# Kernel optimization log

Measured on AMD Instinct MI355X. Metric: run time of the kernel, lower is better.

Reference implementation:

```python
import jax, jax.numpy as jnp
import numpy as np

N = 100000   # num_nodes
F_IN = 128   # num_features
D = 64       # encoder_dim
E = 1600000  # num raw edges (avg degree 16)
BETA = 0.01  # perturb_value


def setup_inputs() -> dict:
    key = jax.random.key(0)
    ks = jax.random.split(key, 8)
    x = jax.random.normal(ks[0], (N, F_IN), dtype=jnp.float32)
    edge_index = jax.random.randint(ks[1], (2, E), 0, N, dtype=jnp.int64)
    W1 = jax.random.normal(ks[2], (F_IN, D), dtype=jnp.float32) * 0.05
    b1 = jnp.zeros((D,), dtype=jnp.float32)
    W2 = jax.random.normal(ks[3], (D, D), dtype=jnp.float32) * 0.05
    b2 = jnp.zeros((D,), dtype=jnp.float32)
    # torch FloatTensor(...).normal_(-beta, beta): mean=-beta, std=beta
    perturb1 = jax.random.normal(ks[4], (N, D), dtype=jnp.float32) * BETA - BETA
    perturb2 = jax.random.normal(ks[5], (N, D), dtype=jnp.float32) * BETA - BETA
    return {"x": x, "edge_index": edge_index, "W1": W1, "b1": b1,
            "W2": W2, "b2": b2, "perturb1": perturb1, "perturb2": perturb2}


def _graph_conv(h, src, dst, norm, W, b):
    # linear transform then gather -> weighted message -> scatter-add
    h = h @ W                                  # [N, D]
    msg = h[src] * norm[:, None]               # [E+N, D] irregular gather
    agg = jax.ops.segment_sum(msg, dst, num_segments=N)  # scatter-add
    return agg + b


def reference(x, edge_index, W1, b1, W2, b2, perturb1, perturb2):
    # add self-loops (GCN/PPMI-style propagation with symmetric norm;
    # PPMI edge weights approximated by degree normalization)
    loops = jnp.arange(N, dtype=edge_index.dtype)
    src = jnp.concatenate([edge_index[0], loops])
    dst = jnp.concatenate([edge_index[1], loops])
    deg = jax.ops.segment_sum(jnp.ones_like(dst, dtype=x.dtype), dst, num_segments=N)
    deg = jnp.maximum(deg, 1.0)
    norm = jax.lax.rsqrt(deg[src] * deg[dst])  # [E+N]

    h = _graph_conv(x, src, dst, norm, W1, b1) + perturb1
    h = jax.nn.relu(h)                         # dropout = identity (eval mode)
    h = _graph_conv(h, src, dst, norm, W2, b2) + perturb2
    return h
```

## Files before the change

### kernel.cpp

```cpp
#include <hip/hip_runtime.h>

#define DD 64
#define FIN 128
#define BK 256
#define MAXBUK 512
#define CAP 8192
#define ESCAP 12288
#define EPB 4096

typedef _Float16 half8 __attribute__((ext_vector_type(8)));
typedef _Float16 h2 __attribute__((ext_vector_type(2)));
typedef float f32x4 __attribute__((ext_vector_type(4)));

union U4 { uint4 u; h2 h[4]; };

__global__ __launch_bounds__(256) void k_bucket(const int* __restrict__ src,
                                                const int* __restrict__ dst,
                                                unsigned* __restrict__ buf,
                                                int* __restrict__ gcur,
                                                int E, int nbuk) {
    __shared__ int hist[MAXBUK];
    __shared__ int base[MAXBUK];
    int e0 = blockIdx.x * EPB;
    int e1 = min(e0 + EPB, E);
    int dreg[16];
#pragma unroll
    for (int i = 0; i < 16; ++i) {
        int e = e0 + threadIdx.x + i * 256;
        dreg[i] = (e < e1) ? dst[e] : -1;
    }
    for (int i = threadIdx.x; i < nbuk; i += 256) hist[i] = 0;
    __syncthreads();
#pragma unroll
    for (int i = 0; i < 16; ++i)
        if (dreg[i] >= 0) atomicAdd(&hist[dreg[i] >> 8], 1);
    __syncthreads();
    for (int i = threadIdx.x; i < nbuk; i += 256) {
        int c = hist[i];
        base[i] = c ? atomicAdd(&gcur[i], c) : 0;
        hist[i] = 0;
    }
    __syncthreads();
#pragma unroll
    for (int i = 0; i < 16; ++i) {
        int d = dreg[i];
        if (d >= 0) {
            int e = e0 + threadIdx.x + i * 256;
            int b = d >> 8;
            int off = base[b] + atomicAdd(&hist[b], 1);
            if (off < CAP)
                buf[(size_t)b * CAP + off] = ((unsigned)src[e] << 8) | ((unsigned)d & 255u);
        }
    }
}

__global__ __launch_bounds__(256) void k_csr(const unsigned* __restrict__ buf,
                                             const int* __restrict__ gcur,
                                             int* __restrict__ rowptr,
                                             int* __restrict__ lenp,
                                             float* __restrict__ rs,
                                             int* __restrict__ es, int n, int dummy) {
    __shared__ int cnt[BK];
    __shared__ int excl[BK];
    __shared__ int cur[BK];
    __shared__ int wsum[4];
    int b = blockIdx.x;
    int tid = threadIdx.x;
    int lane = tid & 63, wid = tid >> 6;
    cnt[tid] = 0;
    cur[tid] = 0;
    __syncthreads();
    int count = gcur[b];
    const unsigned* rec = buf + (size_t)b * CAP;
    for (int i = tid; i < count; i += 256)
        atomicAdd(&cnt[rec[i] & (BK - 1)], 1);
    __syncthreads();
    int v = cnt[tid];
    int pv = (v + 15) & ~15;
    int s = pv;
    for (int off = 1; off < 64; off <<= 1) {
        int t = __shfl_up(s, off, 64);
        if (lane >= off) s += t;
    }
    if (lane == 63) wsum[wid] = s;
    __syncthreads();
    int wo = 0;
    for (int w = 0; w < wid; ++w) wo += wsum[w];
    excl[tid] = s - pv + wo;
    __syncthreads();
    int node = b * BK + tid;
    int base = b * ESCAP;
    if (node < n) {
        rowptr[node] = base + excl[tid];
        lenp[node] = pv;
        rs[node] = rsqrtf((float)(v + 1));
    }
    for (int i = tid; i < count; i += 256) {
        unsigned r = rec[i];
        int local = r & (BK - 1);
        int pos = base + excl[local] + atomicAdd(&cur[local], 1);
        es[pos] = (int)(r >> 8);
    }
    int st = base + excl[tid];
    for (int i = v; i < pv; ++i) es[st + i] = dummy;
}

__global__ __launch_bounds__(256) void k_prep(const float* __restrict__ W1,
                                              const float* __restrict__ W2,
                                              _Float16* __restrict__ Wt1,
                                              _Float16* __restrict__ Wt2,
                                              int* __restrict__ gcur) {
    int tid = threadIdx.x;
    gcur[tid] = 0;
    gcur[tid + 256] = 0;
    for (int i = tid; i < FIN * DD; i += 256) {
        int k = i >> 6, c = i & 63;
        Wt1[c * FIN + k] = (_Float16)W1[i];
    }
    for (int i = tid; i < DD * DD; i += 256) {
        int k = i >> 6, c = i & 63;
        Wt2[c * DD + k] = (_Float16)W2[i];
    }
}

__global__ __launch_bounds__(256) void k_gemm1(const float* __restrict__ x,
                                               const _Float16* __restrict__ Wt,
                                               const float* __restrict__ rs,
                                               _Float16* __restrict__ hpf, int n) {
    __shared__ _Float16 sx[64 * 136];
    int row0 = blockIdx.x * 64;
    int tid = threadIdx.x;
    for (int i = tid; i < 2048; i += 256) {
        int r = i >> 5, c = i & 31;
        int row = row0 + r;
        float4 v = make_float4(0.f, 0.f, 0.f, 0.f);
        if (row < n) v = *(const float4*)(x + (size_t)row * FIN + c * 4);
        union { _Float16 h[4]; uint2 u; } t;
        t.h[0] = (_Float16)v.x; t.h[1] = (_Float16)v.y;
        t.h[2] = (_Float16)v.z; t.h[3] = (_Float16)v.w;
        *(uint2*)(sx + r * 136 + c * 4) = t.u;
    }
    __syncthreads();
    int lane = tid & 63, wave = tid >> 6;
    int r15 = lane & 15, g = lane >> 4;
    half8 a[4];
    const _Float16* ap = sx + (wave * 16 + r15) * 136 + g * 8;
#pragma unroll
    for (int kc = 0; kc < 4; ++kc) a[kc] = *(const half8*)(ap + kc * 32);
    half8 bfr[4][4];
    const _Float16* bp = Wt + (size_t)r15 * FIN + g * 8;
#pragma unroll
    for (int ct = 0; ct < 4; ++ct)
#pragma unroll
        for (int kc = 0; kc < 4; ++kc)
            bfr[ct][kc] = *(const half8*)(bp + ct * 16 * FIN + kc * 32);
    f32x4 acc[4] = {{0.f,0.f,0.f,0.f},{0.f,0.f,0.f,0.f},{0.f,0.f,0.f,0.f},{0.f,0.f,0.f,0.f}};
#pragma unroll
    for (int ct = 0; ct < 4; ++ct)
#pragma unroll
        for (int kc = 0; kc < 4; ++kc)
            acc[ct] = __builtin_amdgcn_mfma_f32_16x16x32_f16(a[kc], bfr[ct][kc], acc[ct], 0, 0, 0);
    __syncthreads();
#pragma unroll
    for (int reg = 0; reg < 4; ++reg) {
        int rowl = wave * 16 + g * 4 + reg;
        int row = row0 + rowl;
        float sc = (row < n) ? rs[row] : 0.f;
#pragma unroll
        for (int ct = 0; ct < 4; ++ct)
            sx[rowl * 72 + ct * 16 + r15] = (_Float16)(acc[ct][reg] * sc);
    }
    __syncthreads();
    for (int i = tid; i < 1024; i += 256) {
        int r = i >> 4, q = i & 15;
        uint2 v = *(const uint2*)(sx + r * 72 + q * 4);
        *(uint2*)(hpf + (size_t)(row0 + r) * DD + q * 4) = v;
    }
}

#define GATHER_BODY                                                              \
    int e0 = rowptr[nc];                                                         \
    int len = alive ? lenp[nc] : 0;                                              \
    int nbt = len >> 4;                                                          \
    h2 ac[2][2][4] = {};                                                         \
    {                                                                            \
        U4 t0, t1;                                                               \
        t0.u = hp4[(size_t)nc * 8 + q];                                          \
        t1.u = hp4[(size_t)nc * 8 + q + 4];                                      \
        _Pragma("unroll")                                                        \
        for (int k = 0; k < 4; ++k) { ac[0][0][k] += t0.h[k]; ac[1][0][k] += t1.h[k]; } \
    }                                                                            \
    for (int t = 0; t < nbt; ++t) {                                              \
        uint4 eb = *(const uint4*)(es + e0 + t * 16 + q * 4);                    \
        int jj[16];                                                              \
        _Pragma("unroll")                                                        \
        for (int l = 0; l < 4; ++l) {                                            \
            jj[l]      = __shfl((int)eb.x, l, 4);                                \
            jj[4 + l]  = __shfl((int)eb.y, l, 4);                                \
            jj[8 + l]  = __shfl((int)eb.z, l, 4);                                \
            jj[12 + l] = __shfl((int)eb.w, l, 4);                                \
        }                                                                        \
        _Pragma("unroll")                                                        \
        for (int hb = 0; hb < 2; ++hb) {                                         \
            U4 v0[8], v1[8];                                                     \
            _Pragma("unroll")                                                    \
            for (int m = 0; m < 8; ++m) {                                        \
                size_t bb = (size_t)jj[hb * 8 + m] * 8;                          \
                v0[m].u = hp4[bb + q];                                           \
                v1[m].u = hp4[bb + q + 4];                                       \
            }                                                                    \
            _Pragma("unroll")                                                    \
            for (int m = 0; m < 8; ++m) {                                        \
                _Pragma("unroll")                                                \
                for (int k = 0; k < 4; ++k) {                                    \
                    ac[0][m & 1][k] += v0[m].h[k];                               \
                    ac[1][m & 1][k] += v1[m].h[k];                               \
                }                                                                \
            }                                                                    \
        }                                                                        \
    }                                                                            \
    float F0[8], F1[8];                                                          \
    _Pragma("unroll")                                                            \
    for (int k = 0; k < 4; ++k) {                                                \
        F0[2 * k]     = (float)ac[0][0][k].x + (float)ac[0][1][k].x;             \
        F0[2 * k + 1] = (float)ac[0][0][k].y + (float)ac[0][1][k].y;             \
        F1[2 * k]     = (float)ac[1][0][k].x + (float)ac[1][1][k].x;             \
        F1[2 * k + 1] = (float)ac[1][0][k].y + (float)ac[1][1][k].y;             \
    }

__global__ __launch_bounds__(256) void k_aggemm(const uint4* __restrict__ hp4,
                                                const int* __restrict__ es,
                                                const int* __restrict__ rowptr,
                                                const int* __restrict__ lenp,
                                                const float* __restrict__ rs,
                                                const float* __restrict__ b,
                                                const float* __restrict__ pert,
                                                const _Float16* __restrict__ Wt,
                                                _Float16* __restrict__ hpo, int n) {
    __shared__ _Float16 sx[64 * 72];
    int tid = threadIdx.x;
    int lane = tid & 63, wv = tid >> 6;
    int q = lane & 3, g = lane >> 2;
    int row0 = blockIdx.x * 64;
    int rowl = wv * 16 + g;
    int node = row0 + rowl;
    bool alive = node < n;
    int nc = alive ? node : 0;
    GATHER_BODY
    {
        float r = rs[nc];
        size_t op = (size_t)nc * DD + q * 8;
        float4 p0 = *(const float4*)(pert + op);
        float4 p1 = *(const float4*)(pert + op + 4);
        float4 p2 = *(const float4*)(pert + op + 32);
        float4 p3 = *(const float4*)(pert + op + 36);
        float4 b0 = *(const float4*)(b + q * 8);
        float4 b1 = *(const float4*)(b + q * 8 + 4);
        float4 b2 = *(const float4*)(b + q * 8 + 32);
        float4 b3 = *(const float4*)(b + q * 8 + 36);
        union { _Float16 h[8]; uint4 u; } t0, t1;
        float m = alive ? 1.f : 0.f;
        t0.h[0] = (_Float16)(m * fmaxf(fmaf(r, F0[0], b0.x + p0.x), 0.f));
        t0.h[1] = (_Float16)(m * fmaxf(fmaf(r, F0[1], b0.y + p0.y), 0.f));
        t0.h[2] = (_Float16)(m * fmaxf(fmaf(r, F0[2], b0.z + p0.z), 0.f));
        t0.h[3] = (_Float16)(m * fmaxf(fmaf(r, F0[3], b0.w + p0.w), 0.f));
        t0.h[4] = (_Float16)(m * fmaxf(fmaf(r, F0[4], b1.x + p1.x), 0.f));
        t0.h[5] = (_Float16)(m * fmaxf(fmaf(r, F0[5], b1.y + p1.y), 0.f));
        t0.h[6] = (_Float16)(m * fmaxf(fmaf(r, F0[6], b1.z + p1.z), 0.f));
        t0.h[7] = (_Float16)(m * fmaxf(fmaf(r, F0[7], b1.w + p1.w), 0.f));
        t1.h[0] = (_Float16)(m * fmaxf(fmaf(r, F1[0], b2.x + p2.x), 0.f));
        t1.h[1] = (_Float16)(m * fmaxf(fmaf(r, F1[1], b2.y + p2.y), 0.f));
        t1.h[2] = (_Float16)(m * fmaxf(fmaf(r, F1[2], b2.z + p2.z), 0.f));
        t1.h[3] = (_Float16)(m * fmaxf(fmaf(r, F1[3], b2.w + p2.w), 0.f));
        t1.h[4] = (_Float16)(m * fmaxf(fmaf(r, F1[4], b3.x + p3.x), 0.f));
        t1.h[5] = (_Float16)(m * fmaxf(fmaf(r, F1[5], b3.y + p3.y), 0.f));
        t1.h[6] = (_Float16)(m * fmaxf(fmaf(r, F1[6], b3.z + p3.z), 0.f));
        t1.h[7] = (_Float16)(m * fmaxf(fmaf(r, F1[7], b3.w + p3.w), 0.f));
        *(uint4*)(sx + rowl * 72 + q * 8) = t0.u;
        *(uint4*)(sx + rowl * 72 + q * 8 + 32) = t1.u;
    }
    __syncthreads();
    int r15 = lane & 15, gg = lane >> 4;
    half8 a[2];
    const _Float16* ap = sx + (wv * 16 + r15) * 72 + gg * 8;
#pragma unroll
    for (int kc = 0; kc < 2; ++kc) a[kc] = *(const half8*)(ap + kc * 32);
    half8 bfr[4][2];
    const _Float16* bp = Wt + (size_t)r15 * DD + gg * 8;
#pragma unroll
    for (int ct = 0; ct < 4; ++ct)
#pragma unroll
        for (int kc = 0; kc < 2; ++kc)
            bfr[ct][kc] = *(const half8*)(bp + ct * 16 * DD + kc * 32);
    f32x4 acc[4] = {{0.f,0.f,0.f,0.f},{0.f,0.f,0.f,0.f},{0.f,0.f,0.f,0.f},{0.f,0.f,0.f,0.f}};
#pragma unroll
    for (int ct = 0; ct < 4; ++ct)
#pragma unroll
        for (int kc = 0; kc < 2; ++kc)
            acc[ct] = __builtin_amdgcn_mfma_f32_16x16x32_f16(a[kc], bfr[ct][kc], acc[ct], 0, 0, 0);
    __syncthreads();
#pragma unroll
    for (int reg = 0; reg < 4; ++reg) {
        int rl = wv * 16 + gg * 4 + reg;
        int row = row0 + rl;
        float sc = (row < n) ? rs[row] : 0.f;
#pragma unroll
        for (int ct = 0; ct < 4; ++ct)
            sx[rl * 72 + ct * 16 + r15] = (_Float16)(acc[ct][reg] * sc);
    }
    __syncthreads();
    for (int i = tid; i < 1024; i += 256) {
        int r = i >> 4, qq = i & 15;
        uint2 v = *(const uint2*)(sx + r * 72 + qq * 4);
        *(uint2*)(hpo + (size_t)(row0 + r) * DD + qq * 4) = v;
    }
}

__global__ __launch_bounds__(256) void k_agg2(const uint4* __restrict__ hp4,
                                              const int* __restrict__ es,
                                              const int* __restrict__ rowptr,
                                              const int* __restrict__ lenp,
                                              const float* __restrict__ rs,
                                              const float* __restrict__ b,
                                              const float* __restrict__ pert,
                                              float* __restrict__ outp, int n) {
    int tid = threadIdx.x;
    int lane = tid & 63, wv = tid >> 6;
    int q = lane & 3, g = lane >> 2;
    int node = blockIdx.x * 64 + wv * 16 + g;
    bool alive = node < n;
    int nc = alive ? node : 0;
    GATHER_BODY
    if (alive) {
        float r = rs[nc];
        size_t op = (size_t)nc * DD + q * 8;
        float4 p0 = *(const float4*)(pert + op);
        float4 p1 = *(const float4*)(pert + op + 4);
        float4 p2 = *(const float4*)(pert + op + 32);
        float4 p3 = *(const float4*)(pert + op + 36);
        float4 b0 = *(const float4*)(b + q * 8);
        float4 b1 = *(const float4*)(b + q * 8 + 4);
        float4 b2 = *(const float4*)(b + q * 8 + 32);
        float4 b3 = *(const float4*)(b + q * 8 + 36);
        float4 r0, r1, r2, r3;
        r0.x = fmaf(r, F0[0], b0.x + p0.x);
        r0.y = fmaf(r, F0[1], b0.y + p0.y);
        r0.z = fmaf(r, F0[2], b0.z + p0.z);
        r0.w = fmaf(r, F0[3], b0.w + p0.w);
        r1.x = fmaf(r, F0[4], b1.x + p1.x);
        r1.y = fmaf(r, F0[5], b1.y + p1.y);
        r1.z = fmaf(r, F0[6], b1.z + p1.z);
        r1.w = fmaf(r, F0[7], b1.w + p1.w);
        r2.x = fmaf(r, F1[0], b2.x + p2.x);
        r2.y = fmaf(r, F1[1], b2.y + p2.y);
        r2.z = fmaf(r, F1[2], b2.z + p2.z);
        r2.w = fmaf(r, F1[3], b2.w + p2.w);
        r3.x = fmaf(r, F1[4], b3.x + p3.x);
        r3.y = fmaf(r, F1[5], b3.y + p3.y);
        r3.z = fmaf(r, F1[6], b3.z + p3.z);
        r3.w = fmaf(r, F1[7], b3.w + p3.w);
        *(float4*)(outp + op) = r0;
        *(float4*)(outp + op + 4) = r1;
        *(float4*)(outp + op + 32) = r2;
        *(float4*)(outp + op + 36) = r3;
    }
}

extern "C" void kernel_launch(void* const* d_in, const int* in_sizes, int n_in,
                              void* d_out, int out_size, void* d_ws, size_t ws_size,
                              hipStream_t stream) {
    const float* x  = (const float*)d_in[0];
    const int*   ei = (const int*)d_in[1];
    const float* W1 = (const float*)d_in[2];
    const float* b1 = (const float*)d_in[3];
    const float* W2 = (const float*)d_in[4];
    const float* b2 = (const float*)d_in[5];
    const float* p1 = (const float*)d_in[6];
    const float* p2 = (const float*)d_in[7];
    float* out = (float*)d_out;

    int n = in_sizes[0] / FIN;
    int E = in_sizes[1] / 2;
    const int* src = ei;
    const int* dst = ei + E;
    int nbuk = (n + BK - 1) / BK;
    int gb = (n + 64) / 64;

    char* ws = (char*)d_ws;
    size_t off = 0;
    int* gcur   = (int*)(ws + off); off += sizeof(int) * MAXBUK;
    int* rowptr = (int*)(ws + off); off += sizeof(int) * (size_t)n;
    int* lenp   = (int*)(ws + off); off += sizeof(int) * (size_t)n;
    float* rs   = (float*)(ws + off); off += sizeof(float) * (size_t)n;
    int* es     = (int*)(ws + off); off += sizeof(int) * (size_t)nbuk * ESCAP;
    off = (off + 15) & ~(size_t)15;
    unsigned* buf = (unsigned*)(ws + off);
    off += sizeof(unsigned) * (size_t)nbuk * CAP;
    off = (off + 15) & ~(size_t)15;
    _Float16* hpf = (_Float16*)(ws + off);
    off += (size_t)gb * 64 * DD * 2;
    off = (off + 15) & ~(size_t)15;
    _Float16* hp2 = (_Float16*)(ws + off);
    off += (size_t)gb * 64 * DD * 2;
    off = (off + 15) & ~(size_t)15;
    _Float16* Wt1 = (_Float16*)(ws + off); off += FIN * DD * 2;
    _Float16* Wt2 = (_Float16*)(ws + off); off += DD * DD * 2;

    int bb = (E + EPB - 1) / EPB;
    int ab = (n + 63) / 64;

    k_prep<<<1, 256, 0, stream>>>(W1, W2, Wt1, Wt2, gcur);
    k_bucket<<<bb, 256, 0, stream>>>(src, dst, buf, gcur, E, nbuk);
    k_csr<<<nbuk, 256, 0, stream>>>(buf, gcur, rowptr, lenp, rs, es, n, n);

    k_gemm1<<<gb, 256, 0, stream>>>(x, Wt1, rs, hpf, n);
    k_aggemm<<<gb, 256, 0, stream>>>((const uint4*)hpf, es, rowptr, lenp, rs,
                                     b1, p1, Wt2, hp2, n);
    k_agg2<<<ab, 256, 0, stream>>>((const uint4*)hp2, es, rowptr, lenp, rs,
                                   b2, p2, out, n);
}
```

Baseline: 153.5 us.

## Replace global atomic bucket offsets with per-block histogram and column scan

```diff
diff --git a/kernel.cpp b/kernel.cpp
--- a/kernel.cpp
+++ b/kernel.cpp
@@ -14,40 +14,65 @@
 
 union U4 { uint4 u; h2 h[4]; };
 
+__global__ __launch_bounds__(256) void k_histA(const int* __restrict__ dst,
+                                               int* __restrict__ hist2d,
+                                               int E, int nbuk) {
+    __shared__ int hist[MAXBUK];
+    int e0 = blockIdx.x * EPB;
+    int e1 = min(e0 + EPB, E);
+    for (int i = threadIdx.x; i < MAXBUK; i += 256) hist[i] = 0;
+    __syncthreads();
+    for (int e = e0 + threadIdx.x; e < e1; e += 256)
+        atomicAdd(&hist[dst[e] >> 8], 1);
+    __syncthreads();
+    for (int i = threadIdx.x; i < MAXBUK; i += 256)
+        hist2d[(size_t)blockIdx.x * MAXBUK + i] = hist[i];
+}
+
+__global__ __launch_bounds__(512) void k_scan2(int* __restrict__ hist2d,
+                                               int* __restrict__ gcur, int nb) {
+    int j = threadIdx.x;
+    int acc = 0;
+    int r = 0;
+    for (; r + 8 <= nb; r += 8) {
+        int t[8];
+#pragma unroll
+        for (int i = 0; i < 8; ++i) t[i] = hist2d[(size_t)(r + i) * MAXBUK + j];
+#pragma unroll
+        for (int i = 0; i < 8; ++i) {
+            hist2d[(size_t)(r + i) * MAXBUK + j] = acc;
+            acc += t[i];
+        }
+    }
+    for (; r < nb; ++r) {
+        int t = hist2d[(size_t)r * MAXBUK + j];
+        hist2d[(size_t)r * MAXBUK + j] = acc;
+        acc += t;
+    }
+    gcur[j] = acc;
+}
+
 __global__ __launch_bounds__(256) void k_bucket(const int* __restrict__ src,
                                                 const int* __restrict__ dst,
                                                 unsigned* __restrict__ buf,
-                                                int* __restrict__ gcur,
+                                                const int* __restrict__ hist2d,
                                                 int E, int nbuk) {
-    __shared__ int hist[MAXBUK];
+    __shared__ int cur[MAXBUK];
     __shared__ int base[MAXBUK];
     int e0 = blockIdx.x * EPB;
     int e1 = min(e0 + EPB, E);
-    int dreg[16];
+    for (int i = threadIdx.x; i < MAXBUK; i += 256) {
+        cur[i] = 0;
+        base[i] = hist2d[(size_t)blockIdx.x * MAXBUK + i];
+    }
+    __syncthreads();
 #pragma unroll
     for (int i = 0; i < 16; ++i) {
         int e = e0 + threadIdx.x + i * 256;
-        dreg[i] = (e < e1) ? dst[e] : -1;
-    }
-    for (int i = threadIdx.x; i < nbuk; i += 256) hist[i] = 0;
-    __syncthreads();
-#pragma unroll
-    for (int i = 0; i < 16; ++i)
-        if (dreg[i] >= 0) atomicAdd(&hist[dreg[i] >> 8], 1);
-    __syncthreads();
-    for (int i = threadIdx.x; i < nbuk; i += 256) {
-        int c = hist[i];
-        base[i] = c ? atomicAdd(&gcur[i], c) : 0;
-        hist[i] = 0;
-    }
-    __syncthreads();
-#pragma unroll
-    for (int i = 0; i < 16; ++i) {
-        int d = dreg[i];
-        if (d >= 0) {
-            int e = e0 + threadIdx.x + i * 256;
+        if (e < e1) {
+            int d = dst[e];
             int b = d >> 8;
-            int off = base[b] + atomicAdd(&hist[b], 1);
+            int off = base[b] + atomicAdd(&cur[b], 1);
             if (off < CAP)
                 buf[(size_t)b * CAP + off] = ((unsigned)src[e] << 8) | ((unsigned)d & 255u);
         }
@@ -108,11 +133,8 @@
 __global__ __launch_bounds__(256) void k_prep(const float* __restrict__ W1,
                                               const float* __restrict__ W2,
                                               _Float16* __restrict__ Wt1,
-                                              _Float16* __restrict__ Wt2,
-                                              int* __restrict__ gcur) {
+                                              _Float16* __restrict__ Wt2) {
     int tid = threadIdx.x;
-    gcur[tid] = 0;
-    gcur[tid + 256] = 0;
     for (int i = tid; i < FIN * DD; i += 256) {
         int k = i >> 6, c = i & 63;
         Wt1[c * FIN + k] = (_Float16)W1[i];
@@ -384,6 +406,7 @@
     const int* src = ei;
     const int* dst = ei + E;
     int nbuk = (n + BK - 1) / BK;
+    int nbb = (E + EPB - 1) / EPB;
     int gb = (n + 64) / 64;
 
     char* ws = (char*)d_ws;
@@ -392,6 +415,7 @@
     int* rowptr = (int*)(ws + off); off += sizeof(int) * (size_t)n;
     int* lenp   = (int*)(ws + off); off += sizeof(int) * (size_t)n;
     float* rs   = (float*)(ws + off); off += sizeof(float) * (size_t)n;
+    int* hist2d = (int*)(ws + off); off += sizeof(int) * (size_t)nbb * MAXBUK;
     int* es     = (int*)(ws + off); off += sizeof(int) * (size_t)nbuk * ESCAP;
     off = (off + 15) & ~(size_t)15;
     unsigned* buf = (unsigned*)(ws + off);
@@ -406,11 +430,12 @@
     _Float16* Wt1 = (_Float16*)(ws + off); off += FIN * DD * 2;
     _Float16* Wt2 = (_Float16*)(ws + off); off += DD * DD * 2;
 
-    int bb = (E + EPB - 1) / EPB;
     int ab = (n + 63) / 64;
 
-    k_prep<<<1, 256, 0, stream>>>(W1, W2, Wt1, Wt2, gcur);
-    k_bucket<<<bb, 256, 0, stream>>>(src, dst, buf, gcur, E, nbuk);
+    k_prep<<<1, 256, 0, stream>>>(W1, W2, Wt1, Wt2);
+    k_histA<<<nbb, 256, 0, stream>>>(dst, hist2d, E, nbuk);
+    k_scan2<<<1, 512, 0, stream>>>(hist2d, gcur, nbb);
+    k_bucket<<<nbb, 256, 0, stream>>>(src, dst, buf, hist2d, E, nbuk);
     k_csr<<<nbuk, 256, 0, stream>>>(buf, gcur, rowptr, lenp, rs, es, n, n);
 
     k_gemm1<<<gb, 256, 0, stream>>>(x, Wt1, rs, hpf, n);
```

After: 175.8 us. 1.14x slower.
